# Kernel optimization log

Hardware: AMD Instinct MI355X
Metric: run time of the kernel (lower is better)

## Reference

```python
import jax, jax.numpy as jnp
import numpy as np

B, L, D, DEPTH, FF, VOCAB = 2, 2048, 1024, 4, 4096, 32000

def setup_inputs():
    key = jax.random.key(0)
    ks = jax.random.split(key, 16)
    n = lambda k, s, sc: jax.random.normal(k, s, dtype=jnp.float32) * sc
    sw = 0.01 / float(np.sqrt(D))  # xavier_normal with gain 0.01 on square dims
    return dict(
        tokens=jax.random.randint(ks[0], (B, L), 0, VOCAB),
        emb=n(ks[1], (VOCAB, D), 0.02),
        Wz=n(ks[2], (DEPTH, D, D), sw), bz=jnp.zeros((DEPTH, D)),
        Wza=n(ks[3], (DEPTH, D, D), sw), bza=jnp.zeros((DEPTH, D)),
        Wy=n(ks[4], (DEPTH, D, D), sw), by=jnp.zeros((DEPTH, D)),
        Wya=n(ks[5], (DEPTH, D, D), sw), bya=jnp.zeros((DEPTH, D)),
        lc_re=n(ks[6], (DEPTH, D), 1.0), lc_im=n(ks[7], (DEPTH, D), 1.0),
        g_in=jnp.ones((DEPTH, D)), g_sc=jnp.ones((DEPTH, D)), g_ffn=jnp.ones((DEPTH, D)),
        Wf=n(ks[8], (DEPTH, D, FF), 0.02), bf=jnp.zeros((DEPTH, FF)),
        Wfa=n(ks[9], (DEPTH, D, FF), 0.02), bfa=jnp.zeros((DEPTH, FF)),
        Wfo=n(ks[10], (DEPTH, FF, D), 0.02), bfo=jnp.zeros((DEPTH, D)),
        ln_w=jnp.ones((D,)), ln_b=jnp.zeros((D,)),
        Wout=n(ks[11], (D, VOCAB), 0.02), bout=jnp.zeros((VOCAB,)),
    )

def _silu(x):
    return x * jax.nn.sigmoid(x)

def _rms(x, w, eps=1e-6):
    return x * jax.lax.rsqrt(jnp.mean(x * x, axis=-1, keepdims=True) + eps) * w

def reference(tokens, emb, Wz, bz, Wza, bza, Wy, by, Wya, bya, lc_re, lc_im,
              g_in, g_sc, g_ffn, Wf, bf, Wfa, bfa, Wfo, bfo, ln_w, ln_b, Wout, bout):
    Bq, Lq = tokens.shape
    # Embedding with max_norm=1: torch renorms accessed rows to norm <= 1
    e = emb[tokens]
    nrm = jnp.linalg.norm(e, axis=-1, keepdims=True)
    x = e * jnp.minimum(1.0, 1.0 / jnp.maximum(nrm, 1e-7))
    # Decaying phazor kernel (shared across layers; phazor_angle_scale is a fixed buffer)
    angle = jnp.power(0.001, jnp.linspace(0.0, 1.0, D))
    ln_ph = (1e-5 + 1j * angle).astype(jnp.complex64)      # [D]
    t = jnp.arange(Lq, dtype=jnp.float32)
    ph = jnp.exp(t[:, None] * ln_ph[None, :])              # [L, D] complex
    pf = jnp.fft.fft(ph, n=2 * Lq, axis=0)                 # [2L, D]
    decay = jnp.exp(ln_ph)                                 # [D]
    for i in range(DEPTH):
        # --- SConv sublayer (pre-RMSNorm + residual) ---
        xr = x
        xn = _rms(x, g_sc[i])
        z = (xn @ Wz[i] + bz[i]) * _silu(xn @ Wza[i] + bza[i])
        zf = jnp.fft.fft(z.astype(jnp.complex64), n=2 * Lq, axis=1)
        h = jnp.fft.ifft(zf * pf[None], axis=1)[:, :Lq]    # inner-chunk causal decaying conv
        lc = (lc_re[i] + 1j * lc_im[i]).astype(jnp.complex64)
        h = h + lc[None, None, :] * ph[None] * decay[None, None, :]  # cross-chunk state carry
        y = (_rms(h.real, g_in[i]) @ Wy[i] + by[i]) * _silu(xn @ Wya[i] + bya[i])
        x = xr + y
        # --- FFN SwiGLU sublayer (pre-RMSNorm + residual) ---
        xr = x
        xn = _rms(x, g_ffn[i])
        x = xr + ((xn @ Wf[i] + bf[i]) * _silu(xn @ Wfa[i] + bfa[i])) @ Wfo[i] + bfo[i]
    # Final LayerNorm + vocab projection
    mu = jnp.mean(x, axis=-1, keepdims=True)
    var = jnp.mean((x - mu) ** 2, axis=-1, keepdims=True)
    x = (x - mu) * jax.lax.rsqrt(var + 1e-5) * ln_w + ln_b
    return x @ Wout + bout
```

## Files before the change

kernel.cpp:

```cpp
#include <hip/hip_runtime.h>
#include <math.h>

typedef __attribute__((ext_vector_type(8))) short bf16x8;
typedef __attribute__((ext_vector_type(4))) float f32x4;

#define DEVI __device__ __forceinline__

DEVI short f2bf(float f) {
  unsigned u = __builtin_bit_cast(unsigned, f);
  return (short)((u + 0x7fffu + ((u >> 16) & 1u)) >> 16);
}
DEVI float bf2f(short s) {
  unsigned u = ((unsigned)(unsigned short)s) << 16;
  return __builtin_bit_cast(float, u);
}

DEVI float silu_f(float v) { return v / (1.0f + expf(-v)); }

DEVI void async16(const void* g, void* l) {
  __builtin_amdgcn_global_load_lds(
      (const __attribute__((address_space(1))) void*)g,
      (__attribute__((address_space(3))) void*)l, 16, 0, 0);
}

template <int N>
DEVI void waitvm() { asm volatile("s_waitcnt vmcnt(%0)" ::"i"(N) : "memory"); }
DEVI void barrier_mem() { asm volatile("s_barrier" ::: "memory"); }
DEVI void lgkm0_sb() {
  asm volatile("s_waitcnt lgkmcnt(0)" ::: "memory");
  __builtin_amdgcn_sched_barrier(0);
}

template <int NROWT>
DEVI void tile_map(int* bx, int* by) {
  const int nwg = gridDim.x;
  const int lin = blockIdx.x;
  const int q = nwg >> 3;
  const int wgid = (lin & 7) * q + (lin >> 3);
  *by = wgid % NROWT;
  *bx = wgid / NROWT;
}

#define SWZ(r) ((ks ^ (((r) >> 1) & 3)) << 4)

__global__ __launch_bounds__(512, 2) void gemm8_k(const short* __restrict__ A,
                                                  const short* __restrict__ BT,
                                                  const float* __restrict__ bias,
                                                  float* __restrict__ outp,
                                                  int N, int K) {
  __shared__ __align__(16) char lds[2 * 65536];
  int bx, by;
  tile_map<16>(&bx, &by);
  const int row0 = by << 8, col0 = bx << 8;
  const int t = threadIdx.x, w = t >> 6, lane = t & 63;
  const int wm = w >> 2, wn = w & 3;
  const int lr = lane & 15, ks = lane >> 4;
  f32x4 acc[8][4] = {};

  const int sslot = (t & 3) ^ ((t >> 3) & 3);
  const char* gA = (const char*)A + ((size_t)(row0 + (t >> 2)) * K) * 2 + sslot * 16;
  const char* gB = (const char*)BT + ((size_t)(col0 + (t >> 2)) * K) * 2 + sslot * 16;
  const size_t cstep = (size_t)K << 8;
  const int t16 = t << 4;

  const int nkt = K >> 6;

#define SA8(nb, kt, s)                                                        \
  {                                                                           \
    const size_t co = (size_t)(kt) * 128 + (s) * 64;                          \
    async16(gA + co, (nb) + (s) * 16384 + t16);                               \
    async16(gA + cstep + co, (nb) + (s) * 16384 + 8192 + t16);                \
  }
#define SB8(nb, kt, s)                                                        \
  {                                                                           \
    const size_t co = (size_t)(kt) * 128 + (s) * 64;                          \
    async16(gB + co, (nb) + 32768 + (s) * 16384 + t16);                       \
    async16(gB + cstep + co, (nb) + 32768 + (s) * 16384 + 8192 + t16);        \
  }
#define RB8(s)                                                                \
  _Pragma("unroll") for (int n = 0; n < 4; ++n) {                             \
    const int rb = (wn << 6) + (n << 4) + lr;                                 \
    bfr[n] = *(const bf16x8*)(base + 32768 + (s) * 16384 + rb * 64 + SWZ(rb)); \
  }
#define RA8(s, mh)                                                            \
  _Pragma("unroll") for (int m = 0; m < 4; ++m) {                             \
    const int r = (wm << 7) + (mh) * 64 + (m << 4) + lr;                      \
    af[m] = *(const bf16x8*)(base + (s) * 16384 + r * 64 + SWZ(r));           \
  }
#define MM8(mh)                                                               \
  __builtin_amdgcn_s_setprio(1);                                              \
  _Pragma("unroll") for (int m = 0; m < 4; ++m)                               \
  _Pragma("unroll") for (int n = 0; n < 4; ++n)                               \
      acc[(mh) * 4 + m][n] = __builtin_amdgcn_mfma_f32_16x16x32_bf16(         \
          af[m], bfr[n], acc[(mh) * 4 + m][n], 0, 0, 0);                      \
  __builtin_amdgcn_s_setprio(0);                                              \
  __builtin_amdgcn_sched_barrier(0);

  {
    char* nb = lds;
    SA8(nb, 0, 0); SB8(nb, 0, 0); SA8(nb, 0, 1); SB8(nb, 0, 1);
  }

  for (int kt = 0; kt < nkt; ++kt) {
    const int ktn = kt + 1;
    const char* base = lds + (kt & 1) * 65536;
    char* nb = lds + (ktn & 1) * 65536;
    bf16x8 af[4], bfr[4];
    waitvm<4>();
    barrier_mem();
    if (ktn < nkt) SA8(nb, ktn, 0);
    RB8(0); RA8(0, 0);
    lgkm0_sb();
    MM8(0);
    barrier_mem();
    if (ktn < nkt) SB8(nb, ktn, 0);
    RA8(0, 1);
    lgkm0_sb();
    MM8(1);
    if (ktn < nkt) waitvm<4>();
    else waitvm<0>();
    barrier_mem();
    if (ktn < nkt) SA8(nb, ktn, 1);
    RB8(1); RA8(1, 0);
    lgkm0_sb();
    MM8(0);
    barrier_mem();
    if (ktn < nkt) SB8(nb, ktn, 1);
    RA8(1, 1);
    lgkm0_sb();
    MM8(1);
  }

  const int orow = row0 + (wm << 7) + (ks << 2);
  const int ocol = col0 + (wn << 6) + lr;
#pragma unroll
  for (int mf = 0; mf < 8; ++mf) {
#pragma unroll
    for (int n = 0; n < 4; ++n) {
      const int c = ocol + (n << 4);
      const float bv = bias[c];
#pragma unroll
      for (int i = 0; i < 4; ++i) {
        const int r = orow + (mf << 4) + i;
        outp[(size_t)r * N + c] = acc[mf][n][i] + bv;
      }
    }
  }
#undef SA8
#undef SB8
#undef RB8
#undef RA8
#undef MM8
}

__global__ __launch_bounds__(512, 2) void dual8_k(const short* __restrict__ A,
                                                  const short* __restrict__ BT1,
                                                  const short* __restrict__ BT2,
                                                  const float* __restrict__ bias1,
                                                  const float* __restrict__ bias2,
                                                  short* __restrict__ outp,
                                                  int N, int K) {
  __shared__ __align__(16) char lds[2 * 32768];
  int bx, by;
  tile_map<16>(&bx, &by);
  const int row0 = by << 8, col0 = bx << 7;
  const int t = threadIdx.x, w = t >> 6, lane = t & 63;
  const int wm = w >> 1, wn = w & 1;
  const int lr = lane & 15, ks = lane >> 4;
  f32x4 acc1[4][4] = {}, acc2[4][4] = {};

  const int sslot = (t & 3) ^ ((t >> 3) & 3);
  const char* gA = (const char*)A + ((size_t)(row0 + (t >> 2)) * K) * 2 + sslot * 16;
  const char* gB1 = (const char*)BT1 + ((size_t)(col0 + (t >> 2)) * K) * 2 + sslot * 16;
  const char* gB2 = (const char*)BT2 + ((size_t)(col0 + (t >> 2)) * K) * 2 + sslot * 16;
  const size_t cstep = (size_t)K << 8;
  const int t16 = t << 4;
  const int nkt = K >> 5;

#define SAD(nb, kt)                                                           \
  {                                                                           \
    const size_t co = (size_t)(kt) * 64;                                      \
    async16(gA + co, (nb) + t16);                                             \
    async16(gA + cstep + co, (nb) + 8192 + t16);                              \
  }
#define SB1D(nb, kt) async16(gB1 + (size_t)(kt) * 64, (nb) + 16384 + t16)
#define SB2D(nb, kt) async16(gB2 + (size_t)(kt) * 64, (nb) + 24576 + t16)

  { char* nb = lds; SAD(nb, 0); SB1D(nb, 0); SB2D(nb, 0); }

  for (int kt = 0; kt < nkt; ++kt) {
    const int ktn = kt + 1;
    const char* base = lds + (kt & 1) * 32768;
    char* nb = lds + (ktn & 1) * 32768;
    bf16x8 af[4], bfr[4];
    waitvm<1>();
    barrier_mem();
    if (ktn < nkt) { SAD(nb, ktn); SB1D(nb, ktn); }
#pragma unroll
    for (int n = 0; n < 4; ++n) {
      const int rb = (wn << 6) + (n << 4) + lr;
      bfr[n] = *(const bf16x8*)(base + 16384 + rb * 64 + SWZ(rb));
    }
#pragma unroll
    for (int m = 0; m < 4; ++m) {
      const int r = (wm << 6) + (m << 4) + lr;
      af[m] = *(const bf16x8*)(base + r * 64 + SWZ(r));
    }
    lgkm0_sb();
    __builtin_amdgcn_s_setprio(1);
#pragma unroll
    for (int m = 0; m < 4; ++m)
#pragma unroll
      for (int n = 0; n < 4; ++n)
        acc1[m][n] = __builtin_amdgcn_mfma_f32_16x16x32_bf16(af[m], bfr[n], acc1[m][n], 0, 0, 0);
    __builtin_amdgcn_s_setprio(0);
    __builtin_amdgcn_sched_barrier(0);
    if (ktn < nkt) waitvm<3>();
    else waitvm<0>();
    barrier_mem();
    if (ktn < nkt) SB2D(nb, ktn);
#pragma unroll
    for (int n = 0; n < 4; ++n) {
      const int rb = (wn << 6) + (n << 4) + lr;
      bfr[n] = *(const bf16x8*)(base + 24576 + rb * 64 + SWZ(rb));
    }
    lgkm0_sb();
    __builtin_amdgcn_s_setprio(1);
#pragma unroll
    for (int m = 0; m < 4; ++m)
#pragma unroll
      for (int n = 0; n < 4; ++n)
        acc2[m][n] = __builtin_amdgcn_mfma_f32_16x16x32_bf16(af[m], bfr[n], acc2[m][n], 0, 0, 0);
    __builtin_amdgcn_s_setprio(0);
    __builtin_amdgcn_sched_barrier(0);
  }

  const int orow = row0 + (wm << 6) + (ks << 2);
  const int ocol = col0 + (wn << 6) + lr;
#pragma unroll
  for (int m = 0; m < 4; ++m) {
#pragma unroll
    for (int n = 0; n < 4; ++n) {
      const int c = ocol + (n << 4);
      const float bv1 = bias1[c], bv2 = bias2[c];
#pragma unroll
      for (int i = 0; i < 4; ++i) {
        const int r = orow + (m << 4) + i;
        outp[(size_t)r * N + c] = f2bf((acc1[m][n][i] + bv1) * silu_f(acc2[m][n][i] + bv2));
      }
    }
  }
#undef SAD
#undef SB1D
#undef SB2D
}

template <int MODE, int BM, int BN, int WM, int WN, int NBUF>
__global__ __launch_bounds__(256, 2) void gemm_k(const short* __restrict__ A,
                                                 const short* __restrict__ BT,
                                                 const float* __restrict__ bias,
                                                 void* __restrict__ outp,
                                                 int N, int K) {
  constexpr int MF = WM / 16, NF = WN / 16;
  constexpr int NWN = BN / WN;
  constexpr int PBB = (BM + BN) * 64;
  constexpr int DEPTH = NBUF - 1;
  constexpr int L = (BM + BN) / 64;
  static_assert((BM / WM) * (BN / WN) == 4, "4 waves");
  __shared__ __align__(16) char lds[NBUF * PBB];
  int bx, by;
  tile_map<4096 / BM>(&bx, &by);
  const int row0 = by * BM, col0 = bx * BN;
  const int t = threadIdx.x, w = t >> 6, lane = t & 63;
  const int wr = w / NWN, wc = w % NWN;
  f32x4 acc[MF][NF] = {};

  const int sslot = (t & 3) ^ ((t >> 3) & 3);
  const char* gA0 = (const char*)A + ((size_t)(row0 + (t >> 2)) * K) * 2 + sslot * 16;
  const char* gB0 = (const char*)BT + ((size_t)(col0 + (t >> 2)) * K) * 2 + sslot * 16;
  const size_t ccstep = (size_t)K * 128;
  const int wb = w << 10;
  const int lr = lane & 15, ks = lane >> 4;

  const int NIT = K >> 5;
  auto stage = [&](int buf, int it) {
    char* dst = lds + buf * PBB;
    const size_t io = (size_t)it * 64;
#pragma unroll
    for (int cc = 0; cc < BM / 64; ++cc)
      async16(gA0 + io + cc * ccstep, dst + cc * 4096 + wb);
#pragma unroll
    for (int cc = 0; cc < BN / 64; ++cc)
      async16(gB0 + io + cc * ccstep, dst + BM * 64 + cc * 4096 + wb);
  };

#pragma unroll
  for (int pit = 0; pit < DEPTH; ++pit) stage(pit, pit);

  for (int it = 0; it < NIT; ++it) {
    const int rem = NIT - it;
    if (rem >= DEPTH + 1) waitvm<L * (DEPTH - 1)>();
    else if (rem >= 2) waitvm<L>();
    else waitvm<0>();
    barrier_mem();
    if (it + DEPTH < NIT) stage((it + DEPTH) % NBUF, it + DEPTH);
    const char* base = lds + (it % NBUF) * PBB;
    bf16x8 af[MF], bfr[NF];
#pragma unroll
    for (int m = 0; m < MF; ++m) {
      const int r = wr * WM + m * 16 + lr;
      af[m] = *(const bf16x8*)(base + r * 64 + SWZ(r));
    }
#pragma unroll
    for (int n = 0; n < NF; ++n) {
      const int r = wc * WN + n * 16 + lr;
      bfr[n] = *(const bf16x8*)(base + BM * 64 + r * 64 + SWZ(r));
    }
#pragma unroll
    for (int m = 0; m < MF; ++m)
#pragma unroll
      for (int n = 0; n < NF; ++n)
        acc[m][n] = __builtin_amdgcn_mfma_f32_16x16x32_bf16(af[m], bfr[n], acc[m][n], 0, 0, 0);
    __builtin_amdgcn_sched_barrier(0);
  }

  const int orow = row0 + wr * WM + (ks << 2);
  const int ocol = col0 + wc * WN + lr;
#pragma unroll
  for (int m = 0; m < MF; ++m) {
#pragma unroll
    for (int n = 0; n < NF; ++n) {
      const int c = ocol + (n << 4);
      const float bv = bias[c];
#pragma unroll
      for (int i = 0; i < 4; ++i) {
        const int r = orow + (m << 4) + i;
        const size_t idx = (size_t)r * N + c;
        float v = acc[m][n][i] + bv;
        if (MODE == 0) ((float*)outp)[idx] = v;
        else ((float*)outp)[idx] += v;
      }
    }
  }
}

template <int MODE, int BM, int BN, int WM, int WN, int NBUF>
__global__ __launch_bounds__(256, 2) void gemm2_k(const short* __restrict__ A1,
                                                  const short* __restrict__ A2,
                                                  const short* __restrict__ BT1,
                                                  const short* __restrict__ BT2,
                                                  const float* __restrict__ bias1,
                                                  const float* __restrict__ bias2,
                                                  void* __restrict__ outp,
                                                  int N, int K) {
  constexpr bool DUALA = (MODE == 1);
  constexpr int MF = WM / 16, NF = WN / 16;
  constexpr int NWN = BN / WN;
  constexpr int ABYTES = BM * 64 * (DUALA ? 2 : 1);
  constexpr int PBB = ABYTES + 2 * BN * 64;
  constexpr int DEPTH = NBUF - 1;
  constexpr int L = ((DUALA ? 2 : 1) * BM + 2 * BN) / 64;
  static_assert((BM / WM) * (BN / WN) == 4, "4 waves");
  __shared__ __align__(16) char lds[NBUF * PBB];
  int bx, by;
  tile_map<4096 / BM>(&bx, &by);
  const int row0 = by * BM, col0 = bx * BN;
  const int t = threadIdx.x, w = t >> 6, lane = t & 63;
  const int wr = w / NWN, wc = w % NWN;
  f32x4 acc1[MF][NF] = {}, acc2[MF][NF] = {};

  const int sslot = (t & 3) ^ ((t >> 3) & 3);
  const size_t arow = ((size_t)(row0 + (t >> 2)) * K) * 2 + sslot * 16;
  const size_t brow = ((size_t)(col0 + (t >> 2)) * K) * 2 + sslot * 16;
  const char* gA1 = (const char*)A1 + arow;
  const char* gA2 = (const char*)A2 + arow;
  const char* gB1 = (const char*)BT1 + brow;
  const char* gB2 = (const char*)BT2 + brow;
  const size_t ccstep = (size_t)K * 128;
  const int wb = w << 10;
  const int lr = lane & 15, ks = lane >> 4;

  const int NIT = K >> 5;
  auto stage = [&](int buf, int it) {
    char* dst = lds + buf * PBB;
    const size_t io = (size_t)it * 64;
#pragma unroll
    for (int cc = 0; cc < BM / 64; ++cc) {
      async16(gA1 + io + cc * ccstep, dst + cc * 4096 + wb);
      if constexpr (DUALA)
        async16(gA2 + io + cc * ccstep, dst + BM * 64 + cc * 4096 + wb);
    }
#pragma unroll
    for (int cc = 0; cc < BN / 64; ++cc) {
      async16(gB1 + io + cc * ccstep, dst + ABYTES + cc * 4096 + wb);
      async16(gB2 + io + cc * ccstep, dst + ABYTES + BN * 64 + cc * 4096 + wb);
    }
  };

#pragma unroll
  for (int pit = 0; pit < DEPTH; ++pit) stage(pit, pit);

  for (int it = 0; it < NIT; ++it) {
    const int rem = NIT - it;
    if (rem >= DEPTH + 1) waitvm<L * (DEPTH - 1)>();
    else if (rem >= 2) waitvm<L>();
    else waitvm<0>();
    barrier_mem();
    if (it + DEPTH < NIT) stage((it + DEPTH) % NBUF, it + DEPTH);
    const char* base = lds + (it % NBUF) * PBB;
    bf16x8 af1[MF], af2[MF], bf1[NF], bf2[NF];
#pragma unroll
    for (int m = 0; m < MF; ++m) {
      const int r = wr * WM + m * 16 + lr;
      const int off = r * 64 + SWZ(r);
      af1[m] = *(const bf16x8*)(base + off);
      if constexpr (DUALA) af2[m] = *(const bf16x8*)(base + BM * 64 + off);
    }
#pragma unroll
    for (int n = 0; n < NF; ++n) {
      const int r = wc * WN + n * 16 + lr;
      const int off = r * 64 + SWZ(r);
      bf1[n] = *(const bf16x8*)(base + ABYTES + off);
      bf2[n] = *(const bf16x8*)(base + ABYTES + BN * 64 + off);
    }
#pragma unroll
    for (int m = 0; m < MF; ++m)
#pragma unroll
      for (int n = 0; n < NF; ++n) {
        acc1[m][n] = __builtin_amdgcn_mfma_f32_16x16x32_bf16(af1[m], bf1[n], acc1[m][n], 0, 0, 0);
        acc2[m][n] = __builtin_amdgcn_mfma_f32_16x16x32_bf16(DUALA ? af2[m] : af1[m], bf2[n],
                                                             acc2[m][n], 0, 0, 0);
      }
    __builtin_amdgcn_sched_barrier(0);
  }

  const int orow = row0 + wr * WM + (ks << 2);
  const int ocol = col0 + wc * WN + lr;
#pragma unroll
  for (int m = 0; m < MF; ++m) {
#pragma unroll
    for (int n = 0; n < NF; ++n) {
      const int c = ocol + (n << 4);
      const float bv1 = bias1[c], bv2 = bias2[c];
#pragma unroll
      for (int i = 0; i < 4; ++i) {
        const int r = orow + (m << 4) + i;
        const size_t idx = (size_t)r * N + c;
        const float g = (acc1[m][n][i] + bv1) * silu_f(acc2[m][n][i] + bv2);
        if (MODE == 1) ((float*)outp)[idx] += g;
        else ((short*)outp)[idx] = f2bf(g);
      }
    }
  }
}

__global__ __launch_bounds__(256) void transp_k(const float* __restrict__ W,
                                                short* __restrict__ WT,
                                                int R, int C) {
  __shared__ float tile[32][33];
  const size_t moff = (size_t)blockIdx.z * R * C;
  const float* Wp = W + moff;
  short* Tp = WT + moff;
  const int c0 = blockIdx.x << 5, r0 = blockIdx.y << 5;
  const int tx = threadIdx.x, ty = threadIdx.y;
#pragma unroll
  for (int i = 0; i < 4; ++i)
    tile[ty + 8 * i][tx] = Wp[(size_t)(r0 + ty + 8 * i) * C + (c0 + tx)];
  __syncthreads();
#pragma unroll
  for (int i = 0; i < 4; ++i)
    Tp[(size_t)(c0 + ty + 8 * i) * R + (r0 + tx)] = f2bf(tile[tx][ty + 8 * i]);
}

__global__ __launch_bounds__(256) void embed_k(const int* __restrict__ tok,
                                               const float* __restrict__ emb,
                                               float* __restrict__ x) {
  const int row = blockIdx.x, t = threadIdx.x, w = t >> 6, lane = t & 63;
  const int token = tok[row];
  float4 v = ((const float4*)(emb + (size_t)token * 1024))[t];
  float ss = v.x * v.x + v.y * v.y + v.z * v.z + v.w * v.w;
#pragma unroll
  for (int off = 32; off; off >>= 1) ss += __shfl_xor(ss, off, 64);
  __shared__ float red[4];
  if (lane == 0) red[w] = ss;
  __syncthreads();
  const float nrm = sqrtf(red[0] + red[1] + red[2] + red[3]);
  const float sc = fminf(1.0f, 1.0f / fmaxf(nrm, 1e-7f));
  v.x *= sc; v.y *= sc; v.z *= sc; v.w *= sc;
  ((float4*)(x + (size_t)row * 1024))[t] = v;
}

template <int BF>
__global__ __launch_bounds__(256) void rms_k(const void* __restrict__ xin,
                                             const float* __restrict__ g,
                                             short* __restrict__ o) {
  const int row = blockIdx.x, t = threadIdx.x, w = t >> 6, lane = t & 63;
  float v0, v1, v2, v3;
  if (BF) {
    short4 s = ((const short4*)((const short*)xin + (size_t)row * 1024))[t];
    v0 = bf2f(s.x); v1 = bf2f(s.y); v2 = bf2f(s.z); v3 = bf2f(s.w);
  } else {
    float4 v = ((const float4*)((const float*)xin + (size_t)row * 1024))[t];
    v0 = v.x; v1 = v.y; v2 = v.z; v3 = v.w;
  }
  float ss = v0 * v0 + v1 * v1 + v2 * v2 + v3 * v3;
#pragma unroll
  for (int off = 32; off; off >>= 1) ss += __shfl_xor(ss, off, 64);
  __shared__ float red[4];
  if (lane == 0) red[w] = ss;
  __syncthreads();
  const float sc = rsqrtf((red[0] + red[1] + red[2] + red[3]) * (1.0f / 1024.0f) + 1e-6f);
  float4 gv = ((const float4*)g)[t];
  short4 ov = make_short4(f2bf(v0 * sc * gv.x), f2bf(v1 * sc * gv.y),
                          f2bf(v2 * sc * gv.z), f2bf(v3 * sc * gv.w));
  *(short4*)(o + (size_t)row * 1024 + 4 * t) = ov;
}

__global__ __launch_bounds__(256) void ln_k(const float* __restrict__ x,
                                            const float* __restrict__ lw,
                                            const float* __restrict__ lb,
                                            short* __restrict__ o) {
  const int row = blockIdx.x, t = threadIdx.x, w = t >> 6, lane = t & 63;
  float4 v = ((const float4*)(x + (size_t)row * 1024))[t];
  float s1 = v.x + v.y + v.z + v.w;
  float s2 = v.x * v.x + v.y * v.y + v.z * v.z + v.w * v.w;
#pragma unroll
  for (int off = 32; off; off >>= 1) {
    s1 += __shfl_xor(s1, off, 64);
    s2 += __shfl_xor(s2, off, 64);
  }
  __shared__ float red[8];
  if (lane == 0) { red[w] = s1; red[4 + w] = s2; }
  __syncthreads();
  const float mu = (red[0] + red[1] + red[2] + red[3]) * (1.0f / 1024.0f);
  const float ex2 = (red[4] + red[5] + red[6] + red[7]) * (1.0f / 1024.0f);
  const float rs = rsqrtf(ex2 - mu * mu + 1e-5f);
  float4 wv = ((const float4*)lw)[t];
  float4 bv = ((const float4*)lb)[t];
  short4 ov = make_short4(f2bf((v.x - mu) * rs * wv.x + bv.x),
                          f2bf((v.y - mu) * rs * wv.y + bv.y),
                          f2bf((v.z - mu) * rs * wv.z + bv.z),
                          f2bf((v.w - mu) * rs * wv.w + bv.w));
  *(short4*)(o + (size_t)row * 1024 + 4 * t) = ov;
}

DEVI void decay_of(int d, float* dr, float* di) {
  const float ang = powf(1e-3f, (float)d * (1.0f / 1023.0f));
  float sn, cs;
  sincosf(ang, &sn, &cs);
  const float mag = expf(1e-5f);
  *dr = mag * cs; *di = mag * sn;
}

__global__ __launch_bounds__(256) void s1_k(const short* __restrict__ z,
                                            float* __restrict__ Er, float* __restrict__ Ei) {
  const int d = (blockIdx.x << 8) + threadIdx.x;
  const int c = blockIdx.y, b = blockIdx.z;
  float dr, di;
  decay_of(d, &dr, &di);
  const short* zp = z + ((size_t)(b * 2048 + c * 64) << 10) + d;
  float sr = 0.0f, si = 0.0f;
  for (int k = 0; k < 64; ++k) {
    float zv = bf2f(zp[(size_t)k << 10]);
    float nr = dr * sr - di * si + zv;
    si = dr * si + di * sr;
    sr = nr;
  }
  const int idx = ((b << 5) + c) * 1024 + d;
  Er[idx] = sr; Ei[idx] = si;
}

__global__ __launch_bounds__(256) void s2_k(const float* __restrict__ Er,
                                            const float* __restrict__ Ei,
                                            float* __restrict__ Sr, float* __restrict__ Si) {
  const int gid = (blockIdx.x << 8) + threadIdx.x;
  const int b = gid >> 10, d = gid & 1023;
  float dr, di;
  decay_of(d, &dr, &di);
  float ar = dr, ai = di;
#pragma unroll
  for (int q = 0; q < 6; ++q) { float nr = ar * ar - ai * ai; ai = 2.0f * ar * ai; ar = nr; }
  float sr = 0.0f, si = 0.0f;
  for (int c = 0; c < 32; ++c) {
    const int idx = ((b << 5) + c) * 1024 + d;
    Sr[idx] = sr; Si[idx] = si;
    const float er = Er[idx], ei = Ei[idx];
    const float nr = ar * sr - ai * si + er;
    si = ar * si + ai * sr + ei;
    sr = nr;
  }
}

__global__ __launch_bounds__(256) void s3_k(const short* __restrict__ z,
                                            const float* __restrict__ Sr,
                                            const float* __restrict__ Si,
                                            const float* __restrict__ lcre,
                                            const float* __restrict__ lcim,
                                            short* __restrict__ h) {
  const int d = (blockIdx.x << 8) + threadIdx.x;
  const int c = blockIdx.y, b = blockIdx.z;
  float dr, di;
  decay_of(d, &dr, &di);
  float ar = dr, ai = di;
#pragma unroll
  for (int q = 0; q < 6; ++q) { float nr = ar * ar - ai * ai; ai = 2.0f * ar * ai; ar = nr; }
  float wr = 1.0f, wi = 0.0f, br = ar, bi = ai;
  int e = c;
  while (e) {
    if (e & 1) { float nr = wr * br - wi * bi; wi = wr * bi + wi * br; wr = nr; }
    float nb = br * br - bi * bi; bi = 2.0f * br * bi; br = nb;
    e >>= 1;
  }
  { float nr = wr * dr - wi * di; wi = wr * di + wi * dr; wr = nr; }
  const int idx = ((b << 5) + c) * 1024 + d;
  float sr = Sr[idx], si = Si[idx];
  const float lr_ = lcre[d], li_ = lcim[d];
  const size_t base = ((size_t)(b * 2048 + c * 64) << 10) + d;
  for (int k = 0; k < 64; ++k) {
    const float zv = bf2f(z[base + ((size_t)k << 10)]);
    const float nr = dr * sr - di * si + zv;
    si = dr * si + di * sr;
    sr = nr;
    h[base + ((size_t)k << 10)] = f2bf(sr + lr_ * wr - li_ * wi);
    const float nw = wr * dr - wi * di;
    wi = wr * di + wi * dr;
    wr = nw;
  }
}

extern "C" void kernel_launch(void* const* d_in, const int* in_sizes, int n_in,
                              void* d_out, int out_size, void* d_ws, size_t ws_size,
                              hipStream_t stream) {
  const int* tokens = (const int*)d_in[0];
  const float* emb = (const float*)d_in[1];
  const float* Wz = (const float*)d_in[2];
  const float* bz = (const float*)d_in[3];
  const float* Wza = (const float*)d_in[4];
  const float* bza = (const float*)d_in[5];
  const float* Wy = (const float*)d_in[6];
  const float* by = (const float*)d_in[7];
  const float* Wya = (const float*)d_in[8];
  const float* bya = (const float*)d_in[9];
  const float* lc_re = (const float*)d_in[10];
  const float* lc_im = (const float*)d_in[11];
  const float* g_in = (const float*)d_in[12];
  const float* g_sc = (const float*)d_in[13];
  const float* g_ffn = (const float*)d_in[14];
  const float* Wf = (const float*)d_in[15];
  const float* bf = (const float*)d_in[16];
  const float* Wfa = (const float*)d_in[17];
  const float* bfa = (const float*)d_in[18];
  const float* Wfo = (const float*)d_in[19];
  const float* bfo = (const float*)d_in[20];
  const float* ln_w = (const float*)d_in[21];
  const float* ln_b = (const float*)d_in[22];
  const float* Wout = (const float*)d_in[23];
  const float* bout = (const float*)d_in[24];

  char* p = (char*)d_ws;
  float* xb = (float*)p;   p += (size_t)4096 * 1024 * 4;
  short* zb = (short*)p;   p += (size_t)4096 * 1024 * 2;
  short* hb = (short*)p;   p += (size_t)4096 * 1024 * 2;
  float* Er = (float*)p;   p += (size_t)2 * 32 * 1024 * 4;
  float* Ei = (float*)p;   p += (size_t)2 * 32 * 1024 * 4;
  float* Sr = (float*)p;   p += (size_t)2 * 32 * 1024 * 4;
  float* Si = (float*)p;   p += (size_t)2 * 32 * 1024 * 4;
  short* xnb = (short*)p;  p += (size_t)4096 * 1024 * 2;
  short* hnb = (short*)p;  p += (size_t)4096 * 1024 * 2;
  short* gb = (short*)p;   p += (size_t)4096 * 4096 * 2;
  short* WzT = (short*)p;  p += (size_t)4 * 1024 * 1024 * 2;
  short* WzaT = (short*)p; p += (size_t)4 * 1024 * 1024 * 2;
  short* WyT = (short*)p;  p += (size_t)4 * 1024 * 1024 * 2;
  short* WyaT = (short*)p; p += (size_t)4 * 1024 * 1024 * 2;
  short* WfT = (short*)p;  p += (size_t)4 * 1024 * 4096 * 2;
  short* WfaT = (short*)p; p += (size_t)4 * 1024 * 4096 * 2;
  short* WfoT = (short*)p; p += (size_t)4 * 1024 * 4096 * 2;
  short* WoutT = (short*)p; p += (size_t)32000 * 1024 * 2;

  const dim3 tb(32, 8);
  transp_k<<<dim3(32, 32, 4), tb, 0, stream>>>(Wz, WzT, 1024, 1024);
  transp_k<<<dim3(32, 32, 4), tb, 0, stream>>>(Wza, WzaT, 1024, 1024);
  transp_k<<<dim3(32, 32, 4), tb, 0, stream>>>(Wy, WyT, 1024, 1024);
  transp_k<<<dim3(32, 32, 4), tb, 0, stream>>>(Wya, WyaT, 1024, 1024);
  transp_k<<<dim3(128, 32, 4), tb, 0, stream>>>(Wf, WfT, 1024, 4096);
  transp_k<<<dim3(128, 32, 4), tb, 0, stream>>>(Wfa, WfaT, 1024, 4096);
  transp_k<<<dim3(32, 128, 4), tb, 0, stream>>>(Wfo, WfoT, 4096, 1024);
  transp_k<<<dim3(1000, 32, 1), tb, 0, stream>>>(Wout, WoutT, 1024, 32000);

  embed_k<<<4096, 256, 0, stream>>>(tokens, emb, xb);

  for (int i = 0; i < 4; ++i) {
    const size_t dd = (size_t)i * 1024 * 1024;
    const size_t dv = (size_t)i * 1024;
    const size_t dw = (size_t)i * 1024 * 4096;
    const size_t df = (size_t)i * 4096;
    rms_k<0><<<4096, 256, 0, stream>>>(xb, g_sc + dv, xnb);
    gemm2_k<2, 128, 128, 64, 64, 3><<<256, 256, 0, stream>>>(
        xnb, xnb, WzT + dd, WzaT + dd, bz + dv, bza + dv, zb, 1024, 1024);
    s1_k<<<dim3(4, 32, 2), 256, 0, stream>>>(zb, Er, Ei);
    s2_k<<<8, 256, 0, stream>>>(Er, Ei, Sr, Si);
    s3_k<<<dim3(4, 32, 2), 256, 0, stream>>>(zb, Sr, Si, lc_re + dv, lc_im + dv, hb);
    rms_k<1><<<4096, 256, 0, stream>>>(hb, g_in + dv, hnb);
    gemm2_k<1, 64, 128, 32, 64, 3><<<512, 256, 0, stream>>>(
        hnb, xnb, WyT + dd, WyaT + dd, by + dv, bya + dv, xb, 1024, 1024);
    rms_k<0><<<4096, 256, 0, stream>>>(xb, g_ffn + dv, xnb);
    dual8_k<<<512, 512, 0, stream>>>(xnb, WfT + dw, WfaT + dw, bf + df, bfa + df,
                                     gb, 4096, 1024);
    gemm_k<4, 128, 128, 64, 64, 3><<<256, 256, 0, stream>>>(
        gb, WfoT + dw, bfo + dv, xb, 1024, 4096);
  }

  ln_k<<<4096, 256, 0, stream>>>(xb, ln_w, ln_b, xnb);
  gemm8_k<<<2000, 512, 0, stream>>>(xnb, WoutT, bout, (float*)d_out, 32000, 1024);

  (void)in_sizes; (void)n_in; (void)out_size; (void)ws_size;
}
```

Baseline: 1.598 ms.

## Fuse z/za/ya projections into one triple GEMM and fold chunk-scan into s3

Adds a triple_k GEMM that computes the xn@Wz, xn@Wza and xn@Wya products in one pass over the shared A tile. It writes z (gated) and the raw ya pre-activation, so the later Wy GEMM becomes a single GEMM whose epilogue applies the silu(ya) gate. The s2 sequential chunk-scan kernel is removed; each s3 block recomputes its prefix state from Er/Ei, and the FFN down-projection switches to 64x128 tiles with 4 buffers and MFMA priority hints. The aim is fewer launches and less repeated reading of A and weights, at the cost of an extra bf16 ya buffer and redundant prefix work in s3.

```diff
diff --git a/kernel.cpp b/kernel.cpp
--- a/kernel.cpp
+++ b/kernel.cpp
@@ -255,10 +255,131 @@
 #undef SB2D
 }
 
+__global__ __launch_bounds__(256, 2) void triple_k(const short* __restrict__ A,
+                                                   const short* __restrict__ BT1,
+                                                   const short* __restrict__ BT2,
+                                                   const short* __restrict__ BT3,
+                                                   const float* __restrict__ b1,
+                                                   const float* __restrict__ b2,
+                                                   const float* __restrict__ b3,
+                                                   short* __restrict__ zout,
+                                                   short* __restrict__ yaout,
+                                                   int N, int K) {
+  constexpr int PBB = 28672;
+  __shared__ __align__(16) char lds[2 * PBB];
+  int bx, by;
+  tile_map<64>(&bx, &by);
+  const int row0 = by << 6, col0 = bx << 7;
+  const int t = threadIdx.x, w = t >> 6, lane = t & 63;
+  const int wr = w >> 1, wc = w & 1;
+  const int lr = lane & 15, ks = lane >> 4;
+  f32x4 acc1[2][4] = {}, acc2[2][4] = {}, acc3[2][4] = {};
+
+  const int sslot = (t & 3) ^ ((t >> 3) & 3);
+  const char* gA = (const char*)A + ((size_t)(row0 + (t >> 2)) * K) * 2 + sslot * 16;
+  const size_t brow = ((size_t)(col0 + (t >> 2)) * K) * 2 + sslot * 16;
+  const char* gB1 = (const char*)BT1 + brow;
+  const char* gB2 = (const char*)BT2 + brow;
+  const char* gB3 = (const char*)BT3 + brow;
+  const size_t cstep = (size_t)K * 128;
+  const int t16 = t << 4;
+  const int nkt = K >> 5;
+
+#define STA(nb, kt) async16(gA + (size_t)(kt) * 64, (nb) + t16)
+#define STB(nb, kt, gp, off)                                                  \
+  {                                                                           \
+    const size_t co = (size_t)(kt) * 64;                                      \
+    async16((gp) + co, (nb) + (off) + t16);                                   \
+    async16((gp) + cstep + co, (nb) + (off) + 4096 + t16);                    \
+  }
+
+  { char* nb = lds; STA(nb, 0); STB(nb, 0, gB1, 4096); STB(nb, 0, gB2, 12288); STB(nb, 0, gB3, 20480); }
+
+  for (int kt = 0; kt < nkt; ++kt) {
+    const int ktn = kt + 1;
+    const char* base = lds + (kt & 1) * PBB;
+    char* nb = lds + (ktn & 1) * PBB;
+    bf16x8 af[2], bfr[4];
+    waitvm<0>();
+    barrier_mem();
+    if (ktn < nkt) { STA(nb, ktn); STB(nb, ktn, gB1, 4096); }
+#pragma unroll
+    for (int m = 0; m < 2; ++m) {
+      const int r = (wr << 5) + (m << 4) + lr;
+      af[m] = *(const bf16x8*)(base + r * 64 + SWZ(r));
+    }
+#pragma unroll
+    for (int n = 0; n < 4; ++n) {
+      const int rb = (wc << 6) + (n << 4) + lr;
+      bfr[n] = *(const bf16x8*)(base + 4096 + rb * 64 + SWZ(rb));
+    }
+    lgkm0_sb();
+    __builtin_amdgcn_s_setprio(1);
+#pragma unroll
+    for (int m = 0; m < 2; ++m)
+#pragma unroll
+      for (int n = 0; n < 4; ++n)
+        acc1[m][n] = __builtin_amdgcn_mfma_f32_16x16x32_bf16(af[m], bfr[n], acc1[m][n], 0, 0, 0);
+    __builtin_amdgcn_s_setprio(0);
+    __builtin_amdgcn_sched_barrier(0);
+    if (ktn < nkt) STB(nb, ktn, gB2, 12288);
+#pragma unroll
+    for (int n = 0; n < 4; ++n) {
+      const int rb = (wc << 6) + (n << 4) + lr;
+      bfr[n] = *(const bf16x8*)(base + 12288 + rb * 64 + SWZ(rb));
+    }
+    lgkm0_sb();
+    __builtin_amdgcn_s_setprio(1);
+#pragma unroll
+    for (int m = 0; m < 2; ++m)
+#pragma unroll
+      for (int n = 0; n < 4; ++n)
+        acc2[m][n] = __builtin_amdgcn_mfma_f32_16x16x32_bf16(af[m], bfr[n], acc2[m][n], 0, 0, 0);
+    __builtin_amdgcn_s_setprio(0);
+    __builtin_amdgcn_sched_barrier(0);
+    if (ktn < nkt) STB(nb, ktn, gB3, 20480);
+#pragma unroll
+    for (int n = 0; n < 4; ++n) {
+      const int rb = (wc << 6) + (n << 4) + lr;
+      bfr[n] = *(const bf16x8*)(base + 20480 + rb * 64 + SWZ(rb));
+    }
+    lgkm0_sb();
+    __builtin_amdgcn_s_setprio(1);
+#pragma unroll
+    for (int m = 0; m < 2; ++m)
+#pragma unroll
+      for (int n = 0; n < 4; ++n)
+        acc3[m][n] = __builtin_amdgcn_mfma_f32_16x16x32_bf16(af[m], bfr[n], acc3[m][n], 0, 0, 0);
+    __builtin_amdgcn_s_setprio(0);
+    __builtin_amdgcn_sched_barrier(0);
+  }
+
+  const int orow = row0 + (wr << 5) + (ks << 2);
+  const int ocol = col0 + (wc << 6) + lr;
+#pragma unroll
+  for (int m = 0; m < 2; ++m) {
+#pragma unroll
+    for (int n = 0; n < 4; ++n) {
+      const int c = ocol + (n << 4);
+      const float bv1 = b1[c], bv2 = b2[c], bv3 = b3[c];
+#pragma unroll
+      for (int i = 0; i < 4; ++i) {
+        const int r = orow + (m << 4) + i;
+        const size_t idx = (size_t)r * N + c;
+        zout[idx] = f2bf((acc1[m][n][i] + bv1) * silu_f(acc2[m][n][i] + bv2));
+        yaout[idx] = f2bf(acc3[m][n][i] + bv3);
+      }
+    }
+  }
+#undef STA
+#undef STB
+}
+
 template <int MODE, int BM, int BN, int WM, int WN, int NBUF>
 __global__ __launch_bounds__(256, 2) void gemm_k(const short* __restrict__ A,
                                                  const short* __restrict__ BT,
                                                  const float* __restrict__ bias,
+                                                 const short* __restrict__ aux,
                                                  void* __restrict__ outp,
                                                  int N, int K) {
   constexpr int MF = WM / 16, NF = WN / 16;
@@ -316,11 +437,14 @@
       const int r = wc * WN + n * 16 + lr;
       bfr[n] = *(const bf16x8*)(base + BM * 64 + r * 64 + SWZ(r));
     }
+    lgkm0_sb();
+    __builtin_amdgcn_s_setprio(1);
 #pragma unroll
     for (int m = 0; m < MF; ++m)
 #pragma unroll
       for (int n = 0; n < NF; ++n)
         acc[m][n] = __builtin_amdgcn_mfma_f32_16x16x32_bf16(af[m], bfr[n], acc[m][n], 0, 0, 0);
+    __builtin_amdgcn_s_setprio(0);
     __builtin_amdgcn_sched_barrier(0);
   }
 
@@ -338,117 +462,8 @@
         const size_t idx = (size_t)r * N + c;
         float v = acc[m][n][i] + bv;
         if (MODE == 0) ((float*)outp)[idx] = v;
+        else if (MODE == 3) ((float*)outp)[idx] += v * silu_f(bf2f(aux[idx]));
         else ((float*)outp)[idx] += v;
-      }
-    }
-  }
-}
-
-template <int MODE, int BM, int BN, int WM, int WN, int NBUF>
-__global__ __launch_bounds__(256, 2) void gemm2_k(const short* __restrict__ A1,
-                                                  const short* __restrict__ A2,
-                                                  const short* __restrict__ BT1,
-                                                  const short* __restrict__ BT2,
-                                                  const float* __restrict__ bias1,
-                                                  const float* __restrict__ bias2,
-                                                  void* __restrict__ outp,
-                                                  int N, int K) {
-  constexpr bool DUALA = (MODE == 1);
-  constexpr int MF = WM / 16, NF = WN / 16;
-  constexpr int NWN = BN / WN;
-  constexpr int ABYTES = BM * 64 * (DUALA ? 2 : 1);
-  constexpr int PBB = ABYTES + 2 * BN * 64;
-  constexpr int DEPTH = NBUF - 1;
-  constexpr int L = ((DUALA ? 2 : 1) * BM + 2 * BN) / 64;
-  static_assert((BM / WM) * (BN / WN) == 4, "4 waves");
-  __shared__ __align__(16) char lds[NBUF * PBB];
-  int bx, by;
-  tile_map<4096 / BM>(&bx, &by);
-  const int row0 = by * BM, col0 = bx * BN;
-  const int t = threadIdx.x, w = t >> 6, lane = t & 63;
-  const int wr = w / NWN, wc = w % NWN;
-  f32x4 acc1[MF][NF] = {}, acc2[MF][NF] = {};
-
-  const int sslot = (t & 3) ^ ((t >> 3) & 3);
-  const size_t arow = ((size_t)(row0 + (t >> 2)) * K) * 2 + sslot * 16;
-  const size_t brow = ((size_t)(col0 + (t >> 2)) * K) * 2 + sslot * 16;
-  const char* gA1 = (const char*)A1 + arow;
-  const char* gA2 = (const char*)A2 + arow;
-  const char* gB1 = (const char*)BT1 + brow;
-  const char* gB2 = (const char*)BT2 + brow;
-  const size_t ccstep = (size_t)K * 128;
-  const int wb = w << 10;
-  const int lr = lane & 15, ks = lane >> 4;
-
-  const int NIT = K >> 5;
-  auto stage = [&](int buf, int it) {
-    char* dst = lds + buf * PBB;
-    const size_t io = (size_t)it * 64;
-#pragma unroll
-    for (int cc = 0; cc < BM / 64; ++cc) {
-      async16(gA1 + io + cc * ccstep, dst + cc * 4096 + wb);
-      if constexpr (DUALA)
-        async16(gA2 + io + cc * ccstep, dst + BM * 64 + cc * 4096 + wb);
-    }
-#pragma unroll
-    for (int cc = 0; cc < BN / 64; ++cc) {
-      async16(gB1 + io + cc * ccstep, dst + ABYTES + cc * 4096 + wb);
-      async16(gB2 + io + cc * ccstep, dst + ABYTES + BN * 64 + cc * 4096 + wb);
-    }
-  };
-
-#pragma unroll
-  for (int pit = 0; pit < DEPTH; ++pit) stage(pit, pit);
-
-  for (int it = 0; it < NIT; ++it) {
-    const int rem = NIT - it;
-    if (rem >= DEPTH + 1) waitvm<L * (DEPTH - 1)>();
-    else if (rem >= 2) waitvm<L>();
-    else waitvm<0>();
-    barrier_mem();
-    if (it + DEPTH < NIT) stage((it + DEPTH) % NBUF, it + DEPTH);
-    const char* base = lds + (it % NBUF) * PBB;
-    bf16x8 af1[MF], af2[MF], bf1[NF], bf2[NF];
-#pragma unroll
-    for (int m = 0; m < MF; ++m) {
-      const int r = wr * WM + m * 16 + lr;
-      const int off = r * 64 + SWZ(r);
-      af1[m] = *(const bf16x8*)(base + off);
-      if constexpr (DUALA) af2[m] = *(const bf16x8*)(base + BM * 64 + off);
-    }
-#pragma unroll
-    for (int n = 0; n < NF; ++n) {
-      const int r = wc * WN + n * 16 + lr;
-      const int off = r * 64 + SWZ(r);
-      bf1[n] = *(const bf16x8*)(base + ABYTES + off);
-      bf2[n] = *(const bf16x8*)(base + ABYTES + BN * 64 + off);
-    }
-#pragma unroll
-    for (int m = 0; m < MF; ++m)
-#pragma unroll
-      for (int n = 0; n < NF; ++n) {
-        acc1[m][n] = __builtin_amdgcn_mfma_f32_16x16x32_bf16(af1[m], bf1[n], acc1[m][n], 0, 0, 0);
-        acc2[m][n] = __builtin_amdgcn_mfma_f32_16x16x32_bf16(DUALA ? af2[m] : af1[m], bf2[n],
-                                                             acc2[m][n], 0, 0, 0);
-      }
-    __builtin_amdgcn_sched_barrier(0);
-  }
-
-  const int orow = row0 + wr * WM + (ks << 2);
-  const int ocol = col0 + wc * WN + lr;
-#pragma unroll
-  for (int m = 0; m < MF; ++m) {
-#pragma unroll
-    for (int n = 0; n < NF; ++n) {
-      const int c = ocol + (n << 4);
-      const float bv1 = bias1[c], bv2 = bias2[c];
-#pragma unroll
-      for (int i = 0; i < 4; ++i) {
-        const int r = orow + (m << 4) + i;
-        const size_t idx = (size_t)r * N + c;
-        const float g = (acc1[m][n][i] + bv1) * silu_f(acc2[m][n][i] + bv2);
-        if (MODE == 1) ((float*)outp)[idx] += g;
-        else ((short*)outp)[idx] = f2bf(g);
       }
     }
   }
@@ -570,30 +585,9 @@
   Er[idx] = sr; Ei[idx] = si;
 }
 
-__global__ __launch_bounds__(256) void s2_k(const float* __restrict__ Er,
+__global__ __launch_bounds__(256) void s3_k(const short* __restrict__ z,
+                                            const float* __restrict__ Er,
                                             const float* __restrict__ Ei,
-                                            float* __restrict__ Sr, float* __restrict__ Si) {
-  const int gid = (blockIdx.x << 8) + threadIdx.x;
-  const int b = gid >> 10, d = gid & 1023;
-  float dr, di;
-  decay_of(d, &dr, &di);
-  float ar = dr, ai = di;
-#pragma unroll
-  for (int q = 0; q < 6; ++q) { float nr = ar * ar - ai * ai; ai = 2.0f * ar * ai; ar = nr; }
-  float sr = 0.0f, si = 0.0f;
-  for (int c = 0; c < 32; ++c) {
-    const int idx = ((b << 5) + c) * 1024 + d;
-    Sr[idx] = sr; Si[idx] = si;
-    const float er = Er[idx], ei = Ei[idx];
-    const float nr = ar * sr - ai * si + er;
-    si = ar * si + ai * sr + ei;
-    sr = nr;
-  }
-}
-
-__global__ __launch_bounds__(256) void s3_k(const short* __restrict__ z,
-                                            const float* __restrict__ Sr,
-                                            const float* __restrict__ Si,
                                             const float* __restrict__ lcre,
                                             const float* __restrict__ lcim,
                                             short* __restrict__ h) {
@@ -604,6 +598,14 @@
   float ar = dr, ai = di;
 #pragma unroll
   for (int q = 0; q < 6; ++q) { float nr = ar * ar - ai * ai; ai = 2.0f * ar * ai; ar = nr; }
+  float sr = 0.0f, si = 0.0f;
+  for (int cc = 0; cc < c; ++cc) {
+    const int eidx = ((b << 5) + cc) * 1024 + d;
+    const float er = Er[eidx], ei = Ei[eidx];
+    const float nr = ar * sr - ai * si + er;
+    si = ar * si + ai * sr + ei;
+    sr = nr;
+  }
   float wr = 1.0f, wi = 0.0f, br = ar, bi = ai;
   int e = c;
   while (e) {
@@ -612,8 +614,6 @@
     e >>= 1;
   }
   { float nr = wr * dr - wi * di; wi = wr * di + wi * dr; wr = nr; }
-  const int idx = ((b << 5) + c) * 1024 + d;
-  float sr = Sr[idx], si = Si[idx];
   const float lr_ = lcre[d], li_ = lcim[d];
   const size_t base = ((size_t)(b * 2048 + c * 64) << 10) + d;
   for (int k = 0; k < 64; ++k) {
@@ -661,10 +661,9 @@
   float* xb = (float*)p;   p += (size_t)4096 * 1024 * 4;
   short* zb = (short*)p;   p += (size_t)4096 * 1024 * 2;
   short* hb = (short*)p;   p += (size_t)4096 * 1024 * 2;
+  short* yab = (short*)p;  p += (size_t)4096 * 1024 * 2;
   float* Er = (float*)p;   p += (size_t)2 * 32 * 1024 * 4;
   float* Ei = (float*)p;   p += (size_t)2 * 32 * 1024 * 4;
-  float* Sr = (float*)p;   p += (size_t)2 * 32 * 1024 * 4;
-  float* Si = (float*)p;   p += (size_t)2 * 32 * 1024 * 4;
   short* xnb = (short*)p;  p += (size_t)4096 * 1024 * 2;
   short* hnb = (short*)p;  p += (size_t)4096 * 1024 * 2;
   short* gb = (short*)p;   p += (size_t)4096 * 4096 * 2;
@@ -695,19 +694,18 @@
     const size_t dw = (size_t)i * 1024 * 4096;
     const size_t df = (size_t)i * 4096;
     rms_k<0><<<4096, 256, 0, stream>>>(xb, g_sc + dv, xnb);
-    gemm2_k<2, 128, 128, 64, 64, 3><<<256, 256, 0, stream>>>(
-        xnb, xnb, WzT + dd, WzaT + dd, bz + dv, bza + dv, zb, 1024, 1024);
+    triple_k<<<512, 256, 0, stream>>>(xnb, WzT + dd, WzaT + dd, WyaT + dd,
+                                      bz + dv, bza + dv, bya + dv, zb, yab, 1024, 1024);
     s1_k<<<dim3(4, 32, 2), 256, 0, stream>>>(zb, Er, Ei);
-    s2_k<<<8, 256, 0, stream>>>(Er, Ei, Sr, Si);
-    s3_k<<<dim3(4, 32, 2), 256, 0, stream>>>(zb, Sr, Si, lc_re + dv, lc_im + dv, hb);
+    s3_k<<<dim3(4, 32, 2), 256, 0, stream>>>(zb, Er, Ei, lc_re + dv, lc_im + dv, hb);
     rms_k<1><<<4096, 256, 0, stream>>>(hb, g_in + dv, hnb);
-    gemm2_k<1, 64, 128, 32, 64, 3><<<512, 256, 0, stream>>>(
-        hnb, xnb, WyT + dd, WyaT + dd, by + dv, bya + dv, xb, 1024, 1024);
+    gemm_k<3, 64, 128, 32, 64, 3><<<512, 256, 0, stream>>>(
+        hnb, WyT + dd, by + dv, yab, xb, 1024, 1024);
     rms_k<0><<<4096, 256, 0, stream>>>(xb, g_ffn + dv, xnb);
     dual8_k<<<512, 512, 0, stream>>>(xnb, WfT + dw, WfaT + dw, bf + df, bfa + df,
                                      gb, 4096, 1024);
-    gemm_k<4, 128, 128, 64, 64, 3><<<256, 256, 0, stream>>>(
-        gb, WfoT + dw, bfo + dv, xb, 1024, 4096);
+    gemm_k<4, 64, 128, 32, 64, 4><<<512, 256, 0, stream>>>(
+        gb, WfoT + dw, bfo + dv, nullptr, xb, 1024, 4096);
   }
 
   ln_k<<<4096, 256, 0, stream>>>(xb, ln_w, ln_b, xnb);
```

Result: no change. 1.568 ms (-1.8%).
